# Kernel tuning notes

Measured on AMD Instinct MI355X. Metric: run time of the kernel, lower is better.

Reference implementation:

```python
import jax, jax.numpy as jnp
import numpy as np
from jax import lax

B, T, I, H = 32, 512, 256, 512


def setup_inputs() -> dict:
    key = jax.random.key(0)
    ks = jax.random.split(key, 6)
    s_ih = 1.0 / np.sqrt(I)
    s_hh = 1.0 / np.sqrt(H)
    return {
        "x": jax.random.normal(ks[0], (B, T, I), dtype=jnp.float32),
        "W_ih_f": jax.random.normal(ks[1], (4 * H, I), dtype=jnp.float32) * s_ih,
        "W_hh_f": jax.random.normal(ks[2], (4 * H, H), dtype=jnp.float32) * s_hh,
        "b_f": jnp.zeros((4 * H,), dtype=jnp.float32),
        "W_ih_b": jax.random.normal(ks[3], (4 * H, I), dtype=jnp.float32) * s_ih,
        "W_hh_b": jax.random.normal(ks[4], (4 * H, H), dtype=jnp.float32) * s_hh,
        "b_b": jnp.zeros((4 * H,), dtype=jnp.float32),
    }


def _lstm(x, W_ih, W_hh, b):
    # x: [B, T, I] -> hidden sequence [B, T, H]
    Bx, Tx, _ = x.shape
    Hh = W_hh.shape[1]
    # precompute input projections for all timesteps: [T, B, 4H]
    x_proj = jnp.einsum('bti,gi->tbg', x, W_ih) + b

    def step(carry, xp):
        h, c = carry
        gates = xp + h @ W_hh.T  # [B, 4H]
        i, f, g, o = jnp.split(gates, 4, axis=-1)
        i = jax.nn.sigmoid(i)
        f = jax.nn.sigmoid(f)
        g = jnp.tanh(g)
        o = jax.nn.sigmoid(o)
        c = f * c + i * g
        h = o * jnp.tanh(c)
        return (h, c), h

    h0 = jnp.zeros((Bx, Hh), dtype=x.dtype)
    c0 = jnp.zeros((Bx, Hh), dtype=x.dtype)
    _, hs = lax.scan(step, (h0, c0), x_proj)  # hs: [T, B, H]
    return hs.transpose(1, 0, 2)


def reference(x, W_ih_f, W_hh_f, b_f, W_ih_b, W_hh_b, b_b):
    out_fwd = _lstm(x, W_ih_f, W_hh_f, b_f)                      # [B, T, H]
    x_rev = jnp.flip(x, axis=1)
    out_bwd = jnp.flip(_lstm(x_rev, W_ih_b, W_hh_b, b_b), axis=1)  # [B, T, H]
    return jnp.concatenate((out_fwd, out_bwd), axis=2)           # [B, T, 2H]
```

## Files before the change

kernel.cpp:

```cpp
#include <hip/hip_runtime.h>

#define B_    32
#define T_    512
#define I_    256
#define H_    512
#define PB    16
#define NBLK  32
#define NT    256
#define NSLOT 4
#define HPITCH 34

typedef __attribute__((ext_vector_type(8))) short  short8;
typedef __attribute__((ext_vector_type(4))) float  float4v;

__device__ __forceinline__ unsigned short f2bf(float f) {
    union { float f; unsigned u; } v; v.f = f;
    unsigned r = v.u + 0x7FFFu + ((v.u >> 16) & 1u);
    return (unsigned short)(r >> 16);
}

__device__ __forceinline__ short8 cvt8(const float* p) {
    float4 u = *reinterpret_cast<const float4*>(p);
    float4 v = *reinterpret_cast<const float4*>(p + 4);
    short8 r;
    r[0] = (short)f2bf(u.x); r[1] = (short)f2bf(u.y);
    r[2] = (short)f2bf(u.z); r[3] = (short)f2bf(u.w);
    r[4] = (short)f2bf(v.x); r[5] = (short)f2bf(v.y);
    r[6] = (short)f2bf(v.z); r[7] = (short)f2bf(v.w);
    return r;
}

__device__ __forceinline__ unsigned long long pack4bf(float a, float b, float c, float d) {
    return (unsigned long long)f2bf(a)
         | ((unsigned long long)f2bf(b) << 16)
         | ((unsigned long long)f2bf(c) << 32)
         | ((unsigned long long)f2bf(d) << 48);
}

__device__ __forceinline__ float sigm(float v)  { return 1.0f / (1.0f + __expf(-v)); }
__device__ __forceinline__ float tanhf_(float v){ return 2.0f / (1.0f + __expf(-2.0f * v)) - 1.0f; }

__global__ __launch_bounds__(256) void build_xfrag(const float* __restrict__ x,
                                                   unsigned short* __restrict__ xf) {
    const int t = blockIdx.x, tid = threadIdx.x;
#pragma unroll
    for (int rep = 0; rep < 4; ++rep) {
        const int eidx  = rep * 256 + tid;
        const int chunk = eidx >> 6, lf = eidx & 63;
        const int kstep = chunk >> 1, nh = chunk & 1;
        const int kq = lf >> 4, nm = lf & 15;
        const int b  = nh * 16 + nm;
        const int i0 = kstep * 32 + kq * 8;
        short8 v = cvt8(x + ((size_t)b * T_ + t) * I_ + i0);
        *reinterpret_cast<short8*>(xf + ((size_t)t * 16 + chunk) * 512 + lf * 8) = v;
    }
}

__global__ __launch_bounds__(NT, 1) void bilstm_mfma(
    const float* __restrict__ Wih_f, const float* __restrict__ Whh_f, const float* __restrict__ bias_f,
    const float* __restrict__ Wih_b, const float* __restrict__ Whh_b, const float* __restrict__ bias_b,
    float* __restrict__ out, float* __restrict__ ws) {

    __shared__ __align__(16) char  sAX[16 * 1024];
    __shared__ __align__(16) char  sAH[32 * 1024];
    __shared__ __align__(16) float sHT[B_ * HPITCH];

    const int tid  = threadIdx.x;
    const int lane = tid & 63;
    const int w    = tid >> 6;
    const int d    = blockIdx.x & 1;
    const int pb   = blockIdx.x >> 1;

    const unsigned short* xfrag = (const unsigned short*)ws;
    unsigned long long* hfrag = (unsigned long long*)((char*)ws + (size_t)T_ * 16 * 1024);
    const char* hfrag_b = (const char*)hfrag;
    unsigned* bar = (unsigned*)((char*)hfrag + (size_t)2 * NSLOT * 32 * 1024);

    const float* Wih = d ? Wih_b : Wih_f;
    const float* Whh = d ? Whh_b : Whh_f;
    const float* bia = d ? bias_b : bias_f;

    const int mA  = lane & 15;
    const int kqA = lane >> 4;
    const int gA  = mA & 3;
    const int gr0 = gA * H_ + 32 * pb + 8 * w + (mA >> 2);
    const int gr1 = gr0 + 4;

    short8 wx0[8], wx1[8], wh0[16], wh1[16];
#pragma unroll
    for (int kst = 0; kst < 8; ++kst) {
        wx0[kst] = cvt8(Wih + (size_t)gr0 * I_ + kst * 32 + kqA * 8);
        wx1[kst] = cvt8(Wih + (size_t)gr1 * I_ + kst * 32 + kqA * 8);
    }
#pragma unroll
    for (int kst = 0; kst < 16; ++kst) {
        wh0[kst] = cvt8(Whh + (size_t)gr0 * H_ + kst * 32 + kqA * 8);
        wh1[kst] = cvt8(Whh + (size_t)gr1 * H_ + kst * 32 + kqA * 8);
    }

    const int hid0 = 32 * pb + 8 * w + kqA;
    float4v bq0, bq1;
#pragma unroll
    for (int g = 0; g < 4; ++g) {
        bq0[g] = bia[g * H_ + hid0];
        bq1[g] = bia[g * H_ + hid0 + 4];
    }

    const int pub_b  = tid & 31;
    const int pub_r8 = tid >> 5;
    const unsigned pub_chunkL = pb * 2 + (pub_b >> 4);
    const unsigned pub_lf     = pub_r8 * 16 + (pub_b & 15);

    float c00 = 0.f, c01 = 0.f, c10 = 0.f, c11 = 0.f;
    __syncthreads();

    for (int t = 0; t < T_; ++t) {
        const int tx    = d ? (T_ - 1 - t) : t;
        const int slot  = t & (NSLOT - 1);
        const int pslot = (t - 1) & (NSLOT - 1);

        {
            const char* src = (const char*)xfrag + ((size_t)tx * 16 + w * 4) * 1024 + lane * 16;
            uint4 xbuf[4];
#pragma unroll
            for (int c = 0; c < 4; ++c) xbuf[c] = *reinterpret_cast<const uint4*>(src + c * 1024);
#pragma unroll
            for (int c = 0; c < 4; ++c)
                *reinterpret_cast<uint4*>(sAX + (w * 4 + c) * 1024 + lane * 16) = xbuf[c];
        }

        if (t > 0 && tid == 0) {
            while (__hip_atomic_load(&bar[d * T_ + (t - 1)], __ATOMIC_RELAXED,
                                     __HIP_MEMORY_SCOPE_AGENT) < PB)
                __builtin_amdgcn_s_sleep(1);
        }
        __syncthreads();

        unsigned long long hbuf[16];
        if (t > 0) {
            const char* src = hfrag_b + ((size_t)(d * NSLOT + pslot) * 32 + w * 8) * 1024 + lane * 16;
#pragma unroll
            for (int c = 0; c < 8; ++c) {
                hbuf[2 * c + 0] = __hip_atomic_load((const unsigned long long*)(src + c * 1024),
                                                    __ATOMIC_RELAXED, __HIP_MEMORY_SCOPE_AGENT);
                hbuf[2 * c + 1] = __hip_atomic_load((const unsigned long long*)(src + c * 1024 + 8),
                                                    __ATOMIC_RELAXED, __HIP_MEMORY_SCOPE_AGENT);
            }
        }

        float4v a00 = bq0, a01 = bq0, a10 = bq1, a11 = bq1;
#pragma unroll
        for (int kst = 0; kst < 8; ++kst) {
            short8 f0 = *reinterpret_cast<const short8*>(sAX + (kst * 2 + 0) * 1024 + lane * 16);
            short8 f1 = *reinterpret_cast<const short8*>(sAX + (kst * 2 + 1) * 1024 + lane * 16);
            a00 = __builtin_amdgcn_mfma_f32_16x16x32_bf16(wx0[kst], f0, a00, 0, 0, 0);
            a01 = __builtin_amdgcn_mfma_f32_16x16x32_bf16(wx0[kst], f1, a01, 0, 0, 0);
            a10 = __builtin_amdgcn_mfma_f32_16x16x32_bf16(wx1[kst], f0, a10, 0, 0, 0);
            a11 = __builtin_amdgcn_mfma_f32_16x16x32_bf16(wx1[kst], f1, a11, 0, 0, 0);
        }

        if (t > 0) {
#pragma unroll
            for (int c = 0; c < 8; ++c) {
                char* dst = sAH + (w * 8 + c) * 1024 + lane * 16;
                *reinterpret_cast<unsigned long long*>(dst)     = hbuf[2 * c + 0];
                *reinterpret_cast<unsigned long long*>(dst + 8) = hbuf[2 * c + 1];
            }
        }
        __syncthreads();

        if (t > 0) {
#pragma unroll
            for (int kst = 0; kst < 16; ++kst) {
                short8 f0 = *reinterpret_cast<const short8*>(sAH + (kst * 2 + 0) * 1024 + lane * 16);
                short8 f1 = *reinterpret_cast<const short8*>(sAH + (kst * 2 + 1) * 1024 + lane * 16);
                a00 = __builtin_amdgcn_mfma_f32_16x16x32_bf16(wh0[kst], f0, a00, 0, 0, 0);
                a01 = __builtin_amdgcn_mfma_f32_16x16x32_bf16(wh0[kst], f1, a01, 0, 0, 0);
                a10 = __builtin_amdgcn_mfma_f32_16x16x32_bf16(wh1[kst], f0, a10, 0, 0, 0);
                a11 = __builtin_amdgcn_mfma_f32_16x16x32_bf16(wh1[kst], f1, a11, 0, 0, 0);
            }
        }

        float h00, h01, h10, h11;
        {
            float iv, fv, gv, ov, c;
            iv = sigm(a00[0]); fv = sigm(a00[1]); gv = tanhf_(a00[2]); ov = sigm(a00[3]);
            c = fv * c00 + iv * gv; c00 = c; h00 = ov * tanhf_(c);
            iv = sigm(a01[0]); fv = sigm(a01[1]); gv = tanhf_(a01[2]); ov = sigm(a01[3]);
            c = fv * c01 + iv * gv; c01 = c; h01 = ov * tanhf_(c);
            iv = sigm(a10[0]); fv = sigm(a10[1]); gv = tanhf_(a10[2]); ov = sigm(a10[3]);
            c = fv * c10 + iv * gv; c10 = c; h10 = ov * tanhf_(c);
            iv = sigm(a11[0]); fv = sigm(a11[1]); gv = tanhf_(a11[2]); ov = sigm(a11[3]);
            c = fv * c11 + iv * gv; c11 = c; h11 = ov * tanhf_(c);
        }

        {
            const int hl = 8 * w + kqA;
            const int bn = mA;
            sHT[(bn)      * HPITCH + hl]     = h00;
            sHT[(bn + 16) * HPITCH + hl]     = h01;
            sHT[(bn)      * HPITCH + hl + 4] = h10;
            sHT[(bn + 16) * HPITCH + hl + 4] = h11;
        }
        __syncthreads();

        float2 f01, f23, f45, f67;
        if (tid < 128) {
            const float* rp = sHT + pub_b * HPITCH + 8 * pub_r8;
            f01 = *reinterpret_cast<const float2*>(rp + 0);
            f23 = *reinterpret_cast<const float2*>(rp + 2);
            f45 = *reinterpret_cast<const float2*>(rp + 4);
            f67 = *reinterpret_cast<const float2*>(rp + 6);
            const unsigned long long lo = pack4bf(f01.x, f01.y, f23.x, f23.y);
            const unsigned long long hi = pack4bf(f45.x, f45.y, f67.x, f67.y);
            char* dst = (char*)hfrag + ((size_t)((d * NSLOT + slot) * 32 + pub_chunkL)) * 1024
                      + pub_lf * 16;
            __hip_atomic_store((unsigned long long*)dst,       lo, __ATOMIC_RELAXED, __HIP_MEMORY_SCOPE_AGENT);
            __hip_atomic_store((unsigned long long*)(dst + 8), hi, __ATOMIC_RELAXED, __HIP_MEMORY_SCOPE_AGENT);
        }
        __syncthreads();

        if (tid == 0)
            __hip_atomic_fetch_add(&bar[d * T_ + t], 1u, __ATOMIC_RELAXED,
                                   __HIP_MEMORY_SCOPE_AGENT);

        if (tid < 128) {
            float* op = out + ((size_t)pub_b * T_ + tx) * (2 * H_) + (size_t)d * H_
                      + 32 * pb + 8 * pub_r8;
            *reinterpret_cast<float4*>(op + 0) = make_float4(f01.x, f01.y, f23.x, f23.y);
            *reinterpret_cast<float4*>(op + 4) = make_float4(f45.x, f45.y, f67.x, f67.y);
        }
    }
}

extern "C" void kernel_launch(void* const* d_in, const int* in_sizes, int n_in,
                              void* d_out, int out_size, void* d_ws, size_t ws_size,
                              hipStream_t stream) {
    const float* x     = (const float*)d_in[0];
    const float* Wih_f = (const float*)d_in[1];
    const float* Whh_f = (const float*)d_in[2];
    const float* b_f   = (const float*)d_in[3];
    const float* Wih_b = (const float*)d_in[4];
    const float* Whh_b = (const float*)d_in[5];
    const float* b_b   = (const float*)d_in[6];
    float* out = (float*)d_out;

    const size_t xf_bytes = (size_t)T_ * 16 * 1024;
    const size_t hf_bytes = (size_t)2 * NSLOT * 32 * 1024;
    const size_t bar_bytes = (size_t)2 * T_ * sizeof(unsigned);

    hipMemsetAsync((char*)d_ws + xf_bytes + hf_bytes, 0, bar_bytes, stream);

    hipLaunchKernelGGL(build_xfrag, dim3(T_), dim3(256), 0, stream,
                       x, (unsigned short*)d_ws);

    hipLaunchKernelGGL(bilstm_mfma, dim3(NBLK), dim3(NT), 0, stream,
                       Wih_f, Whh_f, b_f, Wih_b, Whh_b, b_b, out, (float*)d_ws);
}
```

Baseline: 2.423 ms.

## Co-locate each direction's blocks on one XCD and sync through shared L2

```diff
diff --git a/kernel.cpp b/kernel.cpp
--- a/kernel.cpp
+++ b/kernel.cpp
@@ -5,13 +5,14 @@
 #define I_    256
 #define H_    512
 #define PB    16
-#define NBLK  32
+#define NB_LAUNCH 128
 #define NT    256
 #define NSLOT 4
 #define HPITCH 34
 
-typedef __attribute__((ext_vector_type(8))) short  short8;
-typedef __attribute__((ext_vector_type(4))) float  float4v;
+typedef __attribute__((ext_vector_type(8))) short    short8;
+typedef __attribute__((ext_vector_type(4))) float    float4v;
+typedef __attribute__((ext_vector_type(4))) unsigned uint4v;
 
 __device__ __forceinline__ unsigned short f2bf(float f) {
     union { float f; unsigned u; } v; v.f = f;
@@ -40,6 +41,38 @@
 __device__ __forceinline__ float sigm(float v)  { return 1.0f / (1.0f + __expf(-v)); }
 __device__ __forceinline__ float tanhf_(float v){ return 2.0f / (1.0f + __expf(-2.0f * v)) - 1.0f; }
 
+__device__ __forceinline__ void st4_sc0(unsigned* p, unsigned v) {
+    asm volatile("global_store_dword %0, %1, off sc0" :: "v"(p), "v"(v) : "memory");
+}
+__device__ __forceinline__ void st16_sc0(void* p, uint4v v) {
+    asm volatile("global_store_dwordx4 %0, %1, off sc0" :: "v"(p), "v"(v) : "memory");
+}
+__device__ __forceinline__ unsigned ld32_sc0(const void* p) {
+    unsigned r;
+    asm volatile("global_load_dword %0, %1, off sc0\n\ts_waitcnt vmcnt(0)"
+                 : "=v"(r) : "v"(p) : "memory");
+    return r;
+}
+__device__ __forceinline__ void at_add_l2(unsigned* p, unsigned v) {
+    asm volatile("global_atomic_add %0, %1, off" :: "v"(p), "v"(v) : "memory");
+}
+__device__ __forceinline__ void ld_h_8x16_sc0(const char* src, uint4v out[8]) {
+    const char* src2 = src + 4096;
+    asm volatile(
+        "global_load_dwordx4 %0, %[a], off sc0\n\t"
+        "global_load_dwordx4 %1, %[a], off offset:1024 sc0\n\t"
+        "global_load_dwordx4 %2, %[a], off offset:2048 sc0\n\t"
+        "global_load_dwordx4 %3, %[a], off offset:3072 sc0\n\t"
+        "global_load_dwordx4 %4, %[b], off sc0\n\t"
+        "global_load_dwordx4 %5, %[b], off offset:1024 sc0\n\t"
+        "global_load_dwordx4 %6, %[b], off offset:2048 sc0\n\t"
+        "global_load_dwordx4 %7, %[b], off offset:3072 sc0"
+        : "=&v"(out[0]), "=&v"(out[1]), "=&v"(out[2]), "=&v"(out[3]),
+          "=&v"(out[4]), "=&v"(out[5]), "=&v"(out[6]), "=&v"(out[7])
+        : [a]"v"(src), [b]"v"(src2)
+        : "memory");
+}
+
 __global__ __launch_bounds__(256) void build_xfrag(const float* __restrict__ x,
                                                    unsigned short* __restrict__ xf) {
     const int t = blockIdx.x, tid = threadIdx.x;
@@ -64,17 +97,72 @@
     __shared__ __align__(16) char  sAX[16 * 1024];
     __shared__ __align__(16) char  sAH[32 * 1024];
     __shared__ __align__(16) float sHT[B_ * HPITCH];
+    __shared__ int s_role[3];
 
     const int tid  = threadIdx.x;
     const int lane = tid & 63;
     const int w    = tid >> 6;
-    const int d    = blockIdx.x & 1;
-    const int pb   = blockIdx.x >> 1;
 
     const unsigned short* xfrag = (const unsigned short*)ws;
     unsigned long long* hfrag = (unsigned long long*)((char*)ws + (size_t)T_ * 16 * 1024);
     const char* hfrag_b = (const char*)hfrag;
-    unsigned* bar = (unsigned*)((char*)hfrag + (size_t)2 * NSLOT * 32 * 1024);
+    unsigned* bar   = (unsigned*)((char*)hfrag + (size_t)2 * NSLOT * 32 * 1024);
+    unsigned* ctl   = bar + 1024;
+    unsigned* table = bar + 1024 + 64;
+    unsigned* l2bar = bar + 1280;
+
+    if (tid == 0) {
+        unsigned myxcd;
+        asm volatile("s_getreg_b32 %0, hwreg(HW_REG_XCC_ID)" : "=s"(myxcd));
+        myxcd &= 7u;
+        unsigned g = __hip_atomic_fetch_add(&ctl[0], 1u, __ATOMIC_RELAXED, __HIP_MEMORY_SCOPE_AGENT);
+        __hip_atomic_store(&table[g], myxcd, __ATOMIC_RELAXED, __HIP_MEMORY_SCOPE_AGENT);
+        __hip_atomic_fetch_add(&ctl[1], 1u, __ATOMIC_RELEASE, __HIP_MEMORY_SCOPE_AGENT);
+        while (__hip_atomic_load(&ctl[1], __ATOMIC_ACQUIRE, __HIP_MEMORY_SCOPE_AGENT) < NB_LAUNCH)
+            __builtin_amdgcn_s_sleep(8);
+
+        unsigned cnt[8] = {0, 0, 0, 0, 0, 0, 0, 0};
+        int rank = 0;
+        for (int k = 0; k < NB_LAUNCH; ++k) {
+            unsigned e = __hip_atomic_load(&table[k], __ATOMIC_RELAXED, __HIP_MEMORY_SCOPE_AGENT) & 7u;
+            cnt[e]++;
+            if (k < (int)g && e == myxcd) rank++;
+        }
+        int x0 = 0;
+        for (int x = 1; x < 8; ++x) if (cnt[x] > cnt[x0]) x0 = x;
+        int x1 = -1;
+        for (int x = 0; x < 8; ++x) if (x != x0 && (x1 < 0 || cnt[x] > cnt[x1])) x1 = x;
+
+        int l2 = 0, dd = -1, pbb = -1;
+        const bool both_on_x0 = cnt[x0] >= 32;
+        const bool split2     = (cnt[x0] >= 16) && (x1 >= 0 && cnt[x1] >= 16);
+        if (both_on_x0) {
+            l2 = 1;
+            if ((int)myxcd == x0 && rank < 32) { dd = rank >> 4; pbb = rank & 15; }
+        } else if (split2) {
+            l2 = 1;
+            if ((int)myxcd == x0 && rank < 16)      { dd = 0; pbb = rank; }
+            else if ((int)myxcd == x1 && rank < 16) { dd = 1; pbb = rank; }
+        } else {
+            if (g < 32) { dd = (int)(g & 1); pbb = (int)(g >> 1); }
+        }
+        s_role[0] = l2; s_role[1] = dd; s_role[2] = pbb;
+    }
+    __syncthreads();
+    const int l2mode = s_role[0];
+    const int d      = s_role[1];
+    const int pb     = s_role[2];
+    if (d < 0) return;
+
+    if (l2mode && pb == 0) {
+        unsigned* zp = l2bar + d * T_;
+        st4_sc0(zp + tid, 0u);
+        st4_sc0(zp + tid + 256, 0u);
+        asm volatile("s_waitcnt vmcnt(0)" ::: "memory");
+        __syncthreads();
+        if (tid == 0)
+            __hip_atomic_store(&ctl[2 + d], 1u, __ATOMIC_RELEASE, __HIP_MEMORY_SCOPE_AGENT);
+    }
 
     const float* Wih = d ? Wih_b : Wih_f;
     const float* Whh = d ? Whh_b : Whh_f;
@@ -101,9 +189,9 @@
     const int hid0 = 32 * pb + 8 * w + kqA;
     float4v bq0, bq1;
 #pragma unroll
-    for (int g = 0; g < 4; ++g) {
-        bq0[g] = bia[g * H_ + hid0];
-        bq1[g] = bia[g * H_ + hid0 + 4];
+    for (int g2 = 0; g2 < 4; ++g2) {
+        bq0[g2] = bia[g2 * H_ + hid0];
+        bq1[g2] = bia[g2 * H_ + hid0 + 4];
     }
 
     const int pub_b  = tid & 31;
@@ -111,6 +199,13 @@
     const unsigned pub_chunkL = pb * 2 + (pub_b >> 4);
     const unsigned pub_lf     = pub_r8 * 16 + (pub_b & 15);
 
+    if (l2mode) {
+        if (tid == 0) {
+            while (__hip_atomic_load(&ctl[2 + d], __ATOMIC_ACQUIRE, __HIP_MEMORY_SCOPE_AGENT) == 0u)
+                __builtin_amdgcn_s_sleep(2);
+        }
+    }
+
     float c00 = 0.f, c01 = 0.f, c10 = 0.f, c11 = 0.f;
     __syncthreads();
 
@@ -130,21 +225,38 @@
         }
 
         if (t > 0 && tid == 0) {
-            while (__hip_atomic_load(&bar[d * T_ + (t - 1)], __ATOMIC_RELAXED,
-                                     __HIP_MEMORY_SCOPE_AGENT) < PB)
-                __builtin_amdgcn_s_sleep(1);
+            const int idx = d * T_ + (t - 1);
+            if (l2mode) {
+                int sp = 0;
+                for (;;) {
+                    if (ld32_sc0(l2bar + idx) >= PB) break;
+                    if ((++sp & 15) == 0 &&
+                        __hip_atomic_load(&bar[idx], __ATOMIC_RELAXED,
+                                          __HIP_MEMORY_SCOPE_AGENT) >= PB) break;
+                    __builtin_amdgcn_s_sleep(1);
+                }
+            } else {
+                while (__hip_atomic_load(&bar[idx], __ATOMIC_RELAXED,
+                                         __HIP_MEMORY_SCOPE_AGENT) < PB)
+                    __builtin_amdgcn_s_sleep(1);
+            }
         }
         __syncthreads();
 
         unsigned long long hbuf[16];
+        uint4v hb16[8];
         if (t > 0) {
             const char* src = hfrag_b + ((size_t)(d * NSLOT + pslot) * 32 + w * 8) * 1024 + lane * 16;
-#pragma unroll
-            for (int c = 0; c < 8; ++c) {
-                hbuf[2 * c + 0] = __hip_atomic_load((const unsigned long long*)(src + c * 1024),
-                                                    __ATOMIC_RELAXED, __HIP_MEMORY_SCOPE_AGENT);
-                hbuf[2 * c + 1] = __hip_atomic_load((const unsigned long long*)(src + c * 1024 + 8),
-                                                    __ATOMIC_RELAXED, __HIP_MEMORY_SCOPE_AGENT);
+            if (l2mode) {
+                ld_h_8x16_sc0(src, hb16);
+            } else {
+#pragma unroll
+                for (int c = 0; c < 8; ++c) {
+                    hbuf[2 * c + 0] = __hip_atomic_load((const unsigned long long*)(src + c * 1024),
+                                                        __ATOMIC_RELAXED, __HIP_MEMORY_SCOPE_AGENT);
+                    hbuf[2 * c + 1] = __hip_atomic_load((const unsigned long long*)(src + c * 1024 + 8),
+                                                        __ATOMIC_RELAXED, __HIP_MEMORY_SCOPE_AGENT);
+                }
             }
         }
 
@@ -160,11 +272,19 @@
         }
 
         if (t > 0) {
-#pragma unroll
-            for (int c = 0; c < 8; ++c) {
-                char* dst = sAH + (w * 8 + c) * 1024 + lane * 16;
-                *reinterpret_cast<unsigned long long*>(dst)     = hbuf[2 * c + 0];
-                *reinterpret_cast<unsigned long long*>(dst + 8) = hbuf[2 * c + 1];
+            if (l2mode) {
+                asm volatile("s_waitcnt vmcnt(0)" ::: "memory");
+                __builtin_amdgcn_sched_barrier(0);
+#pragma unroll
+                for (int c = 0; c < 8; ++c)
+                    *reinterpret_cast<uint4v*>(sAH + (w * 8 + c) * 1024 + lane * 16) = hb16[c];
+            } else {
+#pragma unroll
+                for (int c = 0; c < 8; ++c) {
+                    char* dst = sAH + (w * 8 + c) * 1024 + lane * 16;
+                    *reinterpret_cast<unsigned long long*>(dst)     = hbuf[2 * c + 0];
+                    *reinterpret_cast<unsigned long long*>(dst + 8) = hbuf[2 * c + 1];
+                }
             }
         }
         __syncthreads();
@@ -215,14 +335,24 @@
             const unsigned long long hi = pack4bf(f45.x, f45.y, f67.x, f67.y);
             char* dst = (char*)hfrag + ((size_t)((d * NSLOT + slot) * 32 + pub_chunkL)) * 1024
                       + pub_lf * 16;
-            __hip_atomic_store((unsigned long long*)dst,       lo, __ATOMIC_RELAXED, __HIP_MEMORY_SCOPE_AGENT);
-            __hip_atomic_store((unsigned long long*)(dst + 8), hi, __ATOMIC_RELAXED, __HIP_MEMORY_SCOPE_AGENT);
-        }
-        __syncthreads();
-
-        if (tid == 0)
+            if (l2mode) {
+                uint4v pv;
+                pv[0] = (unsigned)lo; pv[1] = (unsigned)(lo >> 32);
+                pv[2] = (unsigned)hi; pv[3] = (unsigned)(hi >> 32);
+                st16_sc0(dst, pv);
+                asm volatile("s_waitcnt vmcnt(0)" ::: "memory");
+            } else {
+                __hip_atomic_store((unsigned long long*)dst,       lo, __ATOMIC_RELAXED, __HIP_MEMORY_SCOPE_AGENT);
+                __hip_atomic_store((unsigned long long*)(dst + 8), hi, __ATOMIC_RELAXED, __HIP_MEMORY_SCOPE_AGENT);
+            }
+        }
+        __syncthreads();
+
+        if (tid == 0) {
+            if (l2mode) at_add_l2(l2bar + d * T_ + t, 1u);
             __hip_atomic_fetch_add(&bar[d * T_ + t], 1u, __ATOMIC_RELAXED,
                                    __HIP_MEMORY_SCOPE_AGENT);
+        }
 
         if (tid < 128) {
             float* op = out + ((size_t)pub_b * T_ + tx) * (2 * H_) + (size_t)d * H_
@@ -247,13 +377,13 @@
 
     const size_t xf_bytes = (size_t)T_ * 16 * 1024;
     const size_t hf_bytes = (size_t)2 * NSLOT * 32 * 1024;
-    const size_t bar_bytes = (size_t)2 * T_ * sizeof(unsigned);
-
-    hipMemsetAsync((char*)d_ws + xf_bytes + hf_bytes, 0, bar_bytes, stream);
+    const size_t ctl_bytes = 5120;
+
+    hipMemsetAsync((char*)d_ws + xf_bytes + hf_bytes, 0, ctl_bytes, stream);
 
     hipLaunchKernelGGL(build_xfrag, dim3(T_), dim3(256), 0, stream,
                        x, (unsigned short*)d_ws);
 
-    hipLaunchKernelGGL(bilstm_mfma, dim3(NBLK), dim3(NT), 0, stream,
+    hipLaunchKernelGGL(bilstm_mfma, dim3(NB_LAUNCH), dim3(NT), 0, stream,
                        Wih_f, Whh_f, b_f, Wih_b, Whh_b, b_b, out, (float*)d_ws);
 }
```

Measured after the change: 2.523 ms. 4.1% more time.

## Interleave forward and backward directions within each block to hide barrier latency

Applied to the files above, without the earlier changes.

```diff
diff --git a/kernel.cpp b/kernel.cpp
--- a/kernel.cpp
+++ b/kernel.cpp
@@ -4,14 +4,14 @@
 #define T_    512
 #define I_    256
 #define H_    512
-#define PB    16
 #define NBLK  32
+#define PBF   32
 #define NT    256
 #define NSLOT 4
-#define HPITCH 34
-
-typedef __attribute__((ext_vector_type(8))) short  short8;
-typedef __attribute__((ext_vector_type(4))) float  float4v;
+#define HPITCH 17
+
+typedef __attribute__((ext_vector_type(8))) short    short8;
+typedef __attribute__((ext_vector_type(4))) float    float4v;
 
 __device__ __forceinline__ unsigned short f2bf(float f) {
     union { float f; unsigned u; } v; v.f = f;
@@ -56,6 +56,115 @@
     }
 }
 
+#define PHASE(D, TXV, NTXV, C0, C1, WX, WH, BQ)                                              \
+  {                                                                                          \
+                                                            \
+    _Pragma("unroll")                                                                        \
+    for (int c = 0; c < 4; ++c)                                                              \
+      *reinterpret_cast<uint4*>(sAX + (w * 4 + c) * 1024 + lane * 16) = xpre[c];             \
+                 \
+    {                                                                                        \
+      const char* nsrc = xfrag_b + ((size_t)(NTXV) * 16 + w * 4) * 1024 + lane * 16;         \
+      _Pragma("unroll")                                                                      \
+      for (int c = 0; c < 4; ++c)                                                            \
+        xpre[c] = *reinterpret_cast<const uint4*>(nsrc + c * 1024);                          \
+    }                                                                                        \
+                   \
+    if (t > 0 && tid == 0) {                                                                 \
+      while (__hip_atomic_load(&bar[(D) * T_ + (t - 1)], __ATOMIC_RELAXED,                   \
+                               __HIP_MEMORY_SCOPE_AGENT) < PBF)                              \
+        __builtin_amdgcn_s_sleep(1);                                                         \
+    }                                                                                        \
+    __syncthreads();                                                                \
+                      \
+    unsigned long long hbuf[16];                                                             \
+    if (t > 0) {                                                                             \
+      const char* hsrc = hfrag_b + ((size_t)((D) * NSLOT + pslot) * 32 + w * 8) * 1024       \
+                       + lane * 16;                                                          \
+      _Pragma("unroll")                                                                      \
+      for (int c = 0; c < 8; ++c) {                                                          \
+        hbuf[2 * c + 0] = __hip_atomic_load((const unsigned long long*)(hsrc + c * 1024),    \
+                                            __ATOMIC_RELAXED, __HIP_MEMORY_SCOPE_AGENT);     \
+        hbuf[2 * c + 1] = __hip_atomic_load((const unsigned long long*)(hsrc + c * 1024 + 8),\
+                                            __ATOMIC_RELAXED, __HIP_MEMORY_SCOPE_AGENT);     \
+      }                                                                                      \
+    }                                                                                        \
+                                                                              \
+    float4v a0 = BQ, a1 = BQ;                                                                \
+    _Pragma("unroll")                                                                        \
+    for (int kst = 0; kst < 8; ++kst) {                                                      \
+      short8 f0 = *reinterpret_cast<const short8*>(sAX + (kst * 2 + 0) * 1024 + lane * 16);  \
+      short8 f1 = *reinterpret_cast<const short8*>(sAX + (kst * 2 + 1) * 1024 + lane * 16);  \
+      a0 = __builtin_amdgcn_mfma_f32_16x16x32_bf16(WX[kst], f0, a0, 0, 0, 0);                \
+      a1 = __builtin_amdgcn_mfma_f32_16x16x32_bf16(WX[kst], f1, a1, 0, 0, 0);                \
+    }                                                                                        \
+                                                                     \
+    if (t > 0) {                                                                             \
+      _Pragma("unroll")                                                                      \
+      for (int c = 0; c < 8; ++c) {                                                          \
+        char* hdst = sAH + (w * 8 + c) * 1024 + lane * 16;                                   \
+        *reinterpret_cast<unsigned long long*>(hdst)     = hbuf[2 * c + 0];                  \
+        *reinterpret_cast<unsigned long long*>(hdst + 8) = hbuf[2 * c + 1];                  \
+      }                                                                                      \
+    }                                                                                        \
+    __syncthreads();                                                                \
+                                                                              \
+    if (t > 0) {                                                                             \
+      _Pragma("unroll")                                                                      \
+      for (int kst = 0; kst < 16; ++kst) {                                                   \
+        short8 f0 = *reinterpret_cast<const short8*>(sAH + (kst * 2 + 0) * 1024 + lane * 16);\
+        short8 f1 = *reinterpret_cast<const short8*>(sAH + (kst * 2 + 1) * 1024 + lane * 16);\
+        a0 = __builtin_amdgcn_mfma_f32_16x16x32_bf16(WH[kst], f0, a0, 0, 0, 0);              \
+        a1 = __builtin_amdgcn_mfma_f32_16x16x32_bf16(WH[kst], f1, a1, 0, 0, 0);              \
+      }                                                                                      \
+    }                                                                                        \
+                                              \
+    float h0v, h1v;                                                                          \
+    {                                                                                        \
+      float iv, fv, gv, ov, cc;                                                              \
+      iv = sigm(a0[0]); fv = sigm(a0[1]); gv = tanhf_(a0[2]); ov = sigm(a0[3]);              \
+      cc = fv * (C0) + iv * gv; (C0) = cc; h0v = ov * tanhf_(cc);                            \
+      iv = sigm(a1[0]); fv = sigm(a1[1]); gv = tanhf_(a1[2]); ov = sigm(a1[3]);              \
+      cc = fv * (C1) + iv * gv; (C1) = cc; h1v = ov * tanhf_(cc);                            \
+    }                                                                                        \
+               \
+    {                                                                                        \
+      const int hl = 4 * w + kqA;                                                            \
+      sHT[mA * HPITCH + hl]        = h0v;                                                    \
+      sHT[(mA + 16) * HPITCH + hl] = h1v;                                                    \
+    }                                                                                        \
+    __syncthreads();                                                               \
+                         \
+    float2 f01, f23, f45, f67;                                                               \
+    if (tid < 64) {                                                                          \
+      const float* rp = sHT + pub_b * HPITCH + 8 * pub_r8;                                   \
+      f01 = *reinterpret_cast<const float2*>(rp + 0);                                        \
+      f23 = *reinterpret_cast<const float2*>(rp + 2);                                        \
+      f45 = *reinterpret_cast<const float2*>(rp + 4);                                        \
+      f67 = *reinterpret_cast<const float2*>(rp + 6);                                        \
+      const unsigned long long lo = pack4bf(f01.x, f01.y, f23.x, f23.y);                     \
+      const unsigned long long hi = pack4bf(f45.x, f45.y, f67.x, f67.y);                     \
+      char* pdst = (char*)hfrag + ((size_t)(((D) * NSLOT + slot) * 32 + pub_chunk)) * 1024   \
+                 + pub_lf * 16;                                                              \
+      __hip_atomic_store((unsigned long long*)pdst,       lo, __ATOMIC_RELAXED,              \
+                         __HIP_MEMORY_SCOPE_AGENT);                                          \
+      __hip_atomic_store((unsigned long long*)(pdst + 8), hi, __ATOMIC_RELAXED,              \
+                         __HIP_MEMORY_SCOPE_AGENT);                                          \
+    }                                                                                        \
+    __syncthreads();                    \
+                                                                              \
+    if (tid == 0)                                                                            \
+      __hip_atomic_fetch_add(&bar[(D) * T_ + t], 1u, __ATOMIC_RELAXED,                       \
+                             __HIP_MEMORY_SCOPE_AGENT);                                      \
+                                                    \
+    if (tid < 64) {                                                                          \
+      float* op = out + ((size_t)pub_b * T_ + (TXV)) * (2 * H_) + (size_t)(D) * H_           \
+                + 16 * pb + 8 * pub_r8;                                                      \
+      *reinterpret_cast<float4*>(op + 0) = make_float4(f01.x, f01.y, f23.x, f23.y);          \
+      *reinterpret_cast<float4*>(op + 4) = make_float4(f45.x, f45.y, f67.x, f67.y);          \
+    }                                                                                        \
+  }
+
 __global__ __launch_bounds__(NT, 1) void bilstm_mfma(
     const float* __restrict__ Wih_f, const float* __restrict__ Whh_f, const float* __restrict__ bias_f,
     const float* __restrict__ Wih_b, const float* __restrict__ Whh_b, const float* __restrict__ bias_b,
@@ -68,168 +177,63 @@
     const int tid  = threadIdx.x;
     const int lane = tid & 63;
     const int w    = tid >> 6;
-    const int d    = blockIdx.x & 1;
-    const int pb   = blockIdx.x >> 1;
-
-    const unsigned short* xfrag = (const unsigned short*)ws;
+    const int pb   = blockIdx.x;
+
+    const char* xfrag_b = (const char*)ws;
     unsigned long long* hfrag = (unsigned long long*)((char*)ws + (size_t)T_ * 16 * 1024);
     const char* hfrag_b = (const char*)hfrag;
     unsigned* bar = (unsigned*)((char*)hfrag + (size_t)2 * NSLOT * 32 * 1024);
 
-    const float* Wih = d ? Wih_b : Wih_f;
-    const float* Whh = d ? Whh_b : Whh_f;
-    const float* bia = d ? bias_b : bias_f;
-
     const int mA  = lane & 15;
     const int kqA = lane >> 4;
     const int gA  = mA & 3;
-    const int gr0 = gA * H_ + 32 * pb + 8 * w + (mA >> 2);
-    const int gr1 = gr0 + 4;
-
-    short8 wx0[8], wx1[8], wh0[16], wh1[16];
+    const int gr  = gA * H_ + 16 * pb + 4 * w + (mA >> 2);
+
+    short8 wxF[8], whF[16], wxB[8], whB[16];
 #pragma unroll
     for (int kst = 0; kst < 8; ++kst) {
-        wx0[kst] = cvt8(Wih + (size_t)gr0 * I_ + kst * 32 + kqA * 8);
-        wx1[kst] = cvt8(Wih + (size_t)gr1 * I_ + kst * 32 + kqA * 8);
+        wxF[kst] = cvt8(Wih_f + (size_t)gr * I_ + kst * 32 + kqA * 8);
+        wxB[kst] = cvt8(Wih_b + (size_t)gr * I_ + kst * 32 + kqA * 8);
     }
 #pragma unroll
     for (int kst = 0; kst < 16; ++kst) {
-        wh0[kst] = cvt8(Whh + (size_t)gr0 * H_ + kst * 32 + kqA * 8);
-        wh1[kst] = cvt8(Whh + (size_t)gr1 * H_ + kst * 32 + kqA * 8);
-    }
-
-    const int hid0 = 32 * pb + 8 * w + kqA;
-    float4v bq0, bq1;
-#pragma unroll
-    for (int g = 0; g < 4; ++g) {
-        bq0[g] = bia[g * H_ + hid0];
-        bq1[g] = bia[g * H_ + hid0 + 4];
+        whF[kst] = cvt8(Whh_f + (size_t)gr * H_ + kst * 32 + kqA * 8);
+        whB[kst] = cvt8(Whh_b + (size_t)gr * H_ + kst * 32 + kqA * 8);
+    }
+
+    const int hid0 = 16 * pb + 4 * w + kqA;
+    float4v bqF, bqB;
+#pragma unroll
+    for (int g2 = 0; g2 < 4; ++g2) {
+        bqF[g2] = bias_f[g2 * H_ + hid0];
+        bqB[g2] = bias_b[g2 * H_ + hid0];
     }
 
     const int pub_b  = tid & 31;
     const int pub_r8 = tid >> 5;
-    const unsigned pub_chunkL = pb * 2 + (pub_b >> 4);
-    const unsigned pub_lf     = pub_r8 * 16 + (pub_b & 15);
-
-    float c00 = 0.f, c01 = 0.f, c10 = 0.f, c11 = 0.f;
+    const unsigned pub_chunk = (unsigned)((pb & ~1) + (pub_b >> 4));
+    const unsigned pub_lf    = (unsigned)(((pb & 1) * 2 + pub_r8) * 16 + (pub_b & 15));
+
+    uint4 xpre[4];
+    {
+        const char* nsrc = xfrag_b + ((size_t)0 * 16 + w * 4) * 1024 + lane * 16;
+#pragma unroll
+        for (int c = 0; c < 4; ++c)
+            xpre[c] = *reinterpret_cast<const uint4*>(nsrc + c * 1024);
+    }
+
+    float cF0 = 0.f, cF1 = 0.f, cB0 = 0.f, cB1 = 0.f;
     __syncthreads();
 
     for (int t = 0; t < T_; ++t) {
-        const int tx    = d ? (T_ - 1 - t) : t;
         const int slot  = t & (NSLOT - 1);
         const int pslot = (t - 1) & (NSLOT - 1);
-
-        {
-            const char* src = (const char*)xfrag + ((size_t)tx * 16 + w * 4) * 1024 + lane * 16;
-            uint4 xbuf[4];
-#pragma unroll
-            for (int c = 0; c < 4; ++c) xbuf[c] = *reinterpret_cast<const uint4*>(src + c * 1024);
-#pragma unroll
-            for (int c = 0; c < 4; ++c)
-                *reinterpret_cast<uint4*>(sAX + (w * 4 + c) * 1024 + lane * 16) = xbuf[c];
-        }
-
-        if (t > 0 && tid == 0) {
-            while (__hip_atomic_load(&bar[d * T_ + (t - 1)], __ATOMIC_RELAXED,
-                                     __HIP_MEMORY_SCOPE_AGENT) < PB)
-                __builtin_amdgcn_s_sleep(1);
-        }
-        __syncthreads();
-
-        unsigned long long hbuf[16];
-        if (t > 0) {
-            const char* src = hfrag_b + ((size_t)(d * NSLOT + pslot) * 32 + w * 8) * 1024 + lane * 16;
-#pragma unroll
-            for (int c = 0; c < 8; ++c) {
-                hbuf[2 * c + 0] = __hip_atomic_load((const unsigned long long*)(src + c * 1024),
-                                                    __ATOMIC_RELAXED, __HIP_MEMORY_SCOPE_AGENT);
-                hbuf[2 * c + 1] = __hip_atomic_load((const unsigned long long*)(src + c * 1024 + 8),
-                                                    __ATOMIC_RELAXED, __HIP_MEMORY_SCOPE_AGENT);
-            }
-        }
-
-        float4v a00 = bq0, a01 = bq0, a10 = bq1, a11 = bq1;
-#pragma unroll
-        for (int kst = 0; kst < 8; ++kst) {
-            short8 f0 = *reinterpret_cast<const short8*>(sAX + (kst * 2 + 0) * 1024 + lane * 16);
-            short8 f1 = *reinterpret_cast<const short8*>(sAX + (kst * 2 + 1) * 1024 + lane * 16);
-            a00 = __builtin_amdgcn_mfma_f32_16x16x32_bf16(wx0[kst], f0, a00, 0, 0, 0);
-            a01 = __builtin_amdgcn_mfma_f32_16x16x32_bf16(wx0[kst], f1, a01, 0, 0, 0);
-            a10 = __builtin_amdgcn_mfma_f32_16x16x32_bf16(wx1[kst], f0, a10, 0, 0, 0);
-            a11 = __builtin_amdgcn_mfma_f32_16x16x32_bf16(wx1[kst], f1, a11, 0, 0, 0);
-        }
-
-        if (t > 0) {
-#pragma unroll
-            for (int c = 0; c < 8; ++c) {
-                char* dst = sAH + (w * 8 + c) * 1024 + lane * 16;
-                *reinterpret_cast<unsigned long long*>(dst)     = hbuf[2 * c + 0];
-                *reinterpret_cast<unsigned long long*>(dst + 8) = hbuf[2 * c + 1];
-            }
-        }
-        __syncthreads();
-
-        if (t > 0) {
-#pragma unroll
-            for (int kst = 0; kst < 16; ++kst) {
-                short8 f0 = *reinterpret_cast<const short8*>(sAH + (kst * 2 + 0) * 1024 + lane * 16);
-                short8 f1 = *reinterpret_cast<const short8*>(sAH + (kst * 2 + 1) * 1024 + lane * 16);
-                a00 = __builtin_amdgcn_mfma_f32_16x16x32_bf16(wh0[kst], f0, a00, 0, 0, 0);
-                a01 = __builtin_amdgcn_mfma_f32_16x16x32_bf16(wh0[kst], f1, a01, 0, 0, 0);
-                a10 = __builtin_amdgcn_mfma_f32_16x16x32_bf16(wh1[kst], f0, a10, 0, 0, 0);
-                a11 = __builtin_amdgcn_mfma_f32_16x16x32_bf16(wh1[kst], f1, a11, 0, 0, 0);
-            }
-        }
-
-        float h00, h01, h10, h11;
-        {
-            float iv, fv, gv, ov, c;
-            iv = sigm(a00[0]); fv = sigm(a00[1]); gv = tanhf_(a00[2]); ov = sigm(a00[3]);
-            c = fv * c00 + iv * gv; c00 = c; h00 = ov * tanhf_(c);
-            iv = sigm(a01[0]); fv = sigm(a01[1]); gv = tanhf_(a01[2]); ov = sigm(a01[3]);
-            c = fv * c01 + iv * gv; c01 = c; h01 = ov * tanhf_(c);
-            iv = sigm(a10[0]); fv = sigm(a10[1]); gv = tanhf_(a10[2]); ov = sigm(a10[3]);
-            c = fv * c10 + iv * gv; c10 = c; h10 = ov * tanhf_(c);
-            iv = sigm(a11[0]); fv = sigm(a11[1]); gv = tanhf_(a11[2]); ov = sigm(a11[3]);
-            c = fv * c11 + iv * gv; c11 = c; h11 = ov * tanhf_(c);
-        }
-
-        {
-            const int hl = 8 * w + kqA;
-            const int bn = mA;
-            sHT[(bn)      * HPITCH + hl]     = h00;
-            sHT[(bn + 16) * HPITCH + hl]     = h01;
-            sHT[(bn)      * HPITCH + hl + 4] = h10;
-            sHT[(bn + 16) * HPITCH + hl + 4] = h11;
-        }
-        __syncthreads();
-
-        float2 f01, f23, f45, f67;
-        if (tid < 128) {
-            const float* rp = sHT + pub_b * HPITCH + 8 * pub_r8;
-            f01 = *reinterpret_cast<const float2*>(rp + 0);
-            f23 = *reinterpret_cast<const float2*>(rp + 2);
-            f45 = *reinterpret_cast<const float2*>(rp + 4);
-            f67 = *reinterpret_cast<const float2*>(rp + 6);
-            const unsigned long long lo = pack4bf(f01.x, f01.y, f23.x, f23.y);
-            const unsigned long long hi = pack4bf(f45.x, f45.y, f67.x, f67.y);
-            char* dst = (char*)hfrag + ((size_t)((d * NSLOT + slot) * 32 + pub_chunkL)) * 1024
-                      + pub_lf * 16;
-            __hip_atomic_store((unsigned long long*)dst,       lo, __ATOMIC_RELAXED, __HIP_MEMORY_SCOPE_AGENT);
-            __hip_atomic_store((unsigned long long*)(dst + 8), hi, __ATOMIC_RELAXED, __HIP_MEMORY_SCOPE_AGENT);
-        }
-        __syncthreads();
-
-        if (tid == 0)
-            __hip_atomic_fetch_add(&bar[d * T_ + t], 1u, __ATOMIC_RELAXED,
-                                   __HIP_MEMORY_SCOPE_AGENT);
-
-        if (tid < 128) {
-            float* op = out + ((size_t)pub_b * T_ + tx) * (2 * H_) + (size_t)d * H_
-                      + 32 * pb + 8 * pub_r8;
-            *reinterpret_cast<float4*>(op + 0) = make_float4(f01.x, f01.y, f23.x, f23.y);
-            *reinterpret_cast<float4*>(op + 4) = make_float4(f45.x, f45.y, f67.x, f67.y);
-        }
+        const int txF   = t;
+        const int txB   = T_ - 1 - t;
+        const int txNext = (t + 1 < T_) ? (t + 1) : 0;
+
+        PHASE(0, txF, txB, cF0, cF1, wxF, whF, bqF)
+        PHASE(1, txB, txNext, cB0, cB1, wxB, whB, bqB)
     }
 }
 
@@ -245,8 +249,8 @@
     const float* b_b   = (const float*)d_in[6];
     float* out = (float*)d_out;
 
-    const size_t xf_bytes = (size_t)T_ * 16 * 1024;
-    const size_t hf_bytes = (size_t)2 * NSLOT * 32 * 1024;
+    const size_t xf_bytes  = (size_t)T_ * 16 * 1024;
+    const size_t hf_bytes  = (size_t)2 * NSLOT * 32 * 1024;
     const size_t bar_bytes = (size_t)2 * T_ * sizeof(unsigned);
 
     hipMemsetAsync((char*)d_ws + xf_bytes + hf_bytes, 0, bar_bytes, stream);
```

After: 5.038 ms. 108% more time.

## Move input projection off critical path and load h fragments directly into registers

Applied to the files above, without the earlier changes.

```diff
diff --git a/kernel.cpp b/kernel.cpp
--- a/kernel.cpp
+++ b/kernel.cpp
@@ -40,6 +40,23 @@
 __device__ __forceinline__ float sigm(float v)  { return 1.0f / (1.0f + __expf(-v)); }
 __device__ __forceinline__ float tanhf_(float v){ return 2.0f / (1.0f + __expf(-2.0f * v)) - 1.0f; }
 
+__device__ __forceinline__ void ld_h8(const char* a, short8* o) {
+    const char* b = a + 4096;
+    asm volatile(
+        "global_load_dwordx4 %0, %[pa], off sc0 sc1\n\t"
+        "global_load_dwordx4 %1, %[pa], off offset:1024 sc0 sc1\n\t"
+        "global_load_dwordx4 %2, %[pa], off offset:2048 sc0 sc1\n\t"
+        "global_load_dwordx4 %3, %[pa], off offset:3072 sc0 sc1\n\t"
+        "global_load_dwordx4 %4, %[pb], off sc0 sc1\n\t"
+        "global_load_dwordx4 %5, %[pb], off offset:1024 sc0 sc1\n\t"
+        "global_load_dwordx4 %6, %[pb], off offset:2048 sc0 sc1\n\t"
+        "global_load_dwordx4 %7, %[pb], off offset:3072 sc0 sc1"
+        : "=&v"(o[0]), "=&v"(o[1]), "=&v"(o[2]), "=&v"(o[3]),
+          "=&v"(o[4]), "=&v"(o[5]), "=&v"(o[6]), "=&v"(o[7])
+        : [pa]"v"(a), [pb]"v"(b)
+        : "memory");
+}
+
 __global__ __launch_bounds__(256) void build_xfrag(const float* __restrict__ x,
                                                    unsigned short* __restrict__ xf) {
     const int t = blockIdx.x, tid = threadIdx.x;
@@ -62,7 +79,6 @@
     float* __restrict__ out, float* __restrict__ ws) {
 
     __shared__ __align__(16) char  sAX[16 * 1024];
-    __shared__ __align__(16) char  sAH[32 * 1024];
     __shared__ __align__(16) float sHT[B_ * HPITCH];
 
     const int tid  = threadIdx.x;
@@ -71,7 +87,7 @@
     const int d    = blockIdx.x & 1;
     const int pb   = blockIdx.x >> 1;
 
-    const unsigned short* xfrag = (const unsigned short*)ws;
+    const char* xfrag_b = (const char*)ws;
     unsigned long long* hfrag = (unsigned long long*)((char*)ws + (size_t)T_ * 16 * 1024);
     const char* hfrag_b = (const char*)hfrag;
     unsigned* bar = (unsigned*)((char*)hfrag + (size_t)2 * NSLOT * 32 * 1024);
@@ -111,24 +127,44 @@
     const unsigned pub_chunkL = pb * 2 + (pub_b >> 4);
     const unsigned pub_lf     = pub_r8 * 16 + (pub_b & 15);
 
+    {
+        const int tx0 = d ? (T_ - 1) : 0;
+        const char* src = xfrag_b + ((size_t)tx0 * 16 + w * 4) * 1024 + lane * 16;
+#pragma unroll
+        for (int c = 0; c < 4; ++c) {
+            uint4 v = *reinterpret_cast<const uint4*>(src + c * 1024);
+            *reinterpret_cast<uint4*>(sAX + (w * 4 + c) * 1024 + lane * 16) = v;
+        }
+    }
+    __syncthreads();
+
+    float4v xa00 = bq0, xa01 = bq0, xa10 = bq1, xa11 = bq1;
+#pragma unroll
+    for (int kst = 0; kst < 8; ++kst) {
+        short8 f0 = *reinterpret_cast<const short8*>(sAX + (kst * 2 + 0) * 1024 + lane * 16);
+        short8 f1 = *reinterpret_cast<const short8*>(sAX + (kst * 2 + 1) * 1024 + lane * 16);
+        xa00 = __builtin_amdgcn_mfma_f32_16x16x32_bf16(wx0[kst], f0, xa00, 0, 0, 0);
+        xa01 = __builtin_amdgcn_mfma_f32_16x16x32_bf16(wx0[kst], f1, xa01, 0, 0, 0);
+        xa10 = __builtin_amdgcn_mfma_f32_16x16x32_bf16(wx1[kst], f0, xa10, 0, 0, 0);
+        xa11 = __builtin_amdgcn_mfma_f32_16x16x32_bf16(wx1[kst], f1, xa11, 0, 0, 0);
+    }
+
+    uint4 xpre[4];
+    {
+        const int tx1 = d ? (T_ - 2) : 1;
+        const char* src = xfrag_b + ((size_t)tx1 * 16 + w * 4) * 1024 + lane * 16;
+#pragma unroll
+        for (int c = 0; c < 4; ++c)
+            xpre[c] = *reinterpret_cast<const uint4*>(src + c * 1024);
+    }
+
     float c00 = 0.f, c01 = 0.f, c10 = 0.f, c11 = 0.f;
-    __syncthreads();
 
     for (int t = 0; t < T_; ++t) {
         const int tx    = d ? (T_ - 1 - t) : t;
         const int slot  = t & (NSLOT - 1);
         const int pslot = (t - 1) & (NSLOT - 1);
 
-        {
-            const char* src = (const char*)xfrag + ((size_t)tx * 16 + w * 4) * 1024 + lane * 16;
-            uint4 xbuf[4];
-#pragma unroll
-            for (int c = 0; c < 4; ++c) xbuf[c] = *reinterpret_cast<const uint4*>(src + c * 1024);
-#pragma unroll
-            for (int c = 0; c < 4; ++c)
-                *reinterpret_cast<uint4*>(sAX + (w * 4 + c) * 1024 + lane * 16) = xbuf[c];
-        }
-
         if (t > 0 && tid == 0) {
             while (__hip_atomic_load(&bar[d * T_ + (t - 1)], __ATOMIC_RELAXED,
                                      __HIP_MEMORY_SCOPE_AGENT) < PB)
@@ -136,44 +172,43 @@
         }
         __syncthreads();
 
-        unsigned long long hbuf[16];
+        float4v a00 = xa00, a01 = xa01, a10 = xa10, a11 = xa11;
+
+        short8 hf[32];
         if (t > 0) {
-            const char* src = hfrag_b + ((size_t)(d * NSLOT + pslot) * 32 + w * 8) * 1024 + lane * 16;
-#pragma unroll
-            for (int c = 0; c < 8; ++c) {
-                hbuf[2 * c + 0] = __hip_atomic_load((const unsigned long long*)(src + c * 1024),
-                                                    __ATOMIC_RELAXED, __HIP_MEMORY_SCOPE_AGENT);
-                hbuf[2 * c + 1] = __hip_atomic_load((const unsigned long long*)(src + c * 1024 + 8),
-                                                    __ATOMIC_RELAXED, __HIP_MEMORY_SCOPE_AGENT);
+            const char* hsrc = hfrag_b + ((size_t)(d * NSLOT + pslot) * 32) * 1024 + lane * 16;
+            ld_h8(hsrc,          hf + 0);
+            ld_h8(hsrc +  8192,  hf + 8);
+            ld_h8(hsrc + 16384,  hf + 16);
+            ld_h8(hsrc + 24576,  hf + 24);
+        }
+
+        if (t + 1 < T_) {
+#pragma unroll
+            for (int c = 0; c < 4; ++c)
+                *reinterpret_cast<uint4*>(sAX + (w * 4 + c) * 1024 + lane * 16) = xpre[c];
+        }
+
+        if (t > 0) {
+            __builtin_amdgcn_sched_barrier(0);
+            asm volatile("s_waitcnt vmcnt(16)" ::: "memory");
+            __builtin_amdgcn_sched_barrier(0);
+#pragma unroll
+            for (int kst = 0; kst < 8; ++kst) {
+                short8 f0 = hf[2 * kst + 0];
+                short8 f1 = hf[2 * kst + 1];
+                a00 = __builtin_amdgcn_mfma_f32_16x16x32_bf16(wh0[kst], f0, a00, 0, 0, 0);
+                a01 = __builtin_amdgcn_mfma_f32_16x16x32_bf16(wh0[kst], f1, a01, 0, 0, 0);
+                a10 = __builtin_amdgcn_mfma_f32_16x16x32_bf16(wh1[kst], f0, a10, 0, 0, 0);
+                a11 = __builtin_amdgcn_mfma_f32_16x16x32_bf16(wh1[kst], f1, a11, 0, 0, 0);
             }
-        }
-
-        float4v a00 = bq0, a01 = bq0, a10 = bq1, a11 = bq1;
-#pragma unroll
-        for (int kst = 0; kst < 8; ++kst) {
-            short8 f0 = *reinterpret_cast<const short8*>(sAX + (kst * 2 + 0) * 1024 + lane * 16);
-            short8 f1 = *reinterpret_cast<const short8*>(sAX + (kst * 2 + 1) * 1024 + lane * 16);
-            a00 = __builtin_amdgcn_mfma_f32_16x16x32_bf16(wx0[kst], f0, a00, 0, 0, 0);
-            a01 = __builtin_amdgcn_mfma_f32_16x16x32_bf16(wx0[kst], f1, a01, 0, 0, 0);
-            a10 = __builtin_amdgcn_mfma_f32_16x16x32_bf16(wx1[kst], f0, a10, 0, 0, 0);
-            a11 = __builtin_amdgcn_mfma_f32_16x16x32_bf16(wx1[kst], f1, a11, 0, 0, 0);
-        }
-
-        if (t > 0) {
-#pragma unroll
-            for (int c = 0; c < 8; ++c) {
-                char* dst = sAH + (w * 8 + c) * 1024 + lane * 16;
-                *reinterpret_cast<unsigned long long*>(dst)     = hbuf[2 * c + 0];
-                *reinterpret_cast<unsigned long long*>(dst + 8) = hbuf[2 * c + 1];
-            }
-        }
-        __syncthreads();
-
-        if (t > 0) {
-#pragma unroll
-            for (int kst = 0; kst < 16; ++kst) {
-                short8 f0 = *reinterpret_cast<const short8*>(sAH + (kst * 2 + 0) * 1024 + lane * 16);
-                short8 f1 = *reinterpret_cast<const short8*>(sAH + (kst * 2 + 1) * 1024 + lane * 16);
+            __builtin_amdgcn_sched_barrier(0);
+            asm volatile("s_waitcnt vmcnt(0)" ::: "memory");
+            __builtin_amdgcn_sched_barrier(0);
+#pragma unroll
+            for (int kst = 8; kst < 16; ++kst) {
+                short8 f0 = hf[2 * kst + 0];
+                short8 f1 = hf[2 * kst + 1];
                 a00 = __builtin_amdgcn_mfma_f32_16x16x32_bf16(wh0[kst], f0, a00, 0, 0, 0);
                 a01 = __builtin_amdgcn_mfma_f32_16x16x32_bf16(wh0[kst], f1, a01, 0, 0, 0);
                 a10 = __builtin_amdgcn_mfma_f32_16x16x32_bf16(wh1[kst], f0, a10, 0, 0, 0);
@@ -230,6 +265,27 @@
             *reinterpret_cast<float4*>(op + 0) = make_float4(f01.x, f01.y, f23.x, f23.y);
             *reinterpret_cast<float4*>(op + 4) = make_float4(f45.x, f45.y, f67.x, f67.y);
         }
+
+        if (t + 1 < T_) {
+            xa00 = bq0; xa01 = bq0; xa10 = bq1; xa11 = bq1;
+#pragma unroll
+            for (int kst = 0; kst < 8; ++kst) {
+                short8 f0 = *reinterpret_cast<const short8*>(sAX + (kst * 2 + 0) * 1024 + lane * 16);
+                short8 f1 = *reinterpret_cast<const short8*>(sAX + (kst * 2 + 1) * 1024 + lane * 16);
+                xa00 = __builtin_amdgcn_mfma_f32_16x16x32_bf16(wx0[kst], f0, xa00, 0, 0, 0);
+                xa01 = __builtin_amdgcn_mfma_f32_16x16x32_bf16(wx0[kst], f1, xa01, 0, 0, 0);
+                xa10 = __builtin_amdgcn_mfma_f32_16x16x32_bf16(wx1[kst], f0, xa10, 0, 0, 0);
+                xa11 = __builtin_amdgcn_mfma_f32_16x16x32_bf16(wx1[kst], f1, xa11, 0, 0, 0);
+            }
+        }
+
+        if (t + 2 < T_) {
+            const int txn2 = d ? (T_ - 3 - t) : (t + 2);
+            const char* src = xfrag_b + ((size_t)txn2 * 16 + w * 4) * 1024 + lane * 16;
+#pragma unroll
+            for (int c = 0; c < 4; ++c)
+                xpre[c] = *reinterpret_cast<const uint4*>(src + c * 1024);
+        }
     }
 }
 
@@ -245,8 +301,8 @@
     const float* b_b   = (const float*)d_in[6];
     float* out = (float*)d_out;
 
-    const size_t xf_bytes = (size_t)T_ * 16 * 1024;
-    const size_t hf_bytes = (size_t)2 * NSLOT * 32 * 1024;
+    const size_t xf_bytes  = (size_t)T_ * 16 * 1024;
+    const size_t hf_bytes  = (size_t)2 * NSLOT * 32 * 1024;
     const size_t bar_bytes = (size_t)2 * T_ * sizeof(unsigned);
 
     hipMemsetAsync((char*)d_ws + xf_bytes + hf_bytes, 0, bar_bytes, stream);
```

After: 2.750 ms. 1.13x slower.
